# Kernel optimization log

Hardware: AMD Instinct MI355X
Metric: run time of the kernel (lower is better)

Reference implementation:

```python
import jax, jax.numpy as jnp
import numpy as np

N_NODES = 500_000
N_EDGES = 5_000_000


def setup_inputs() -> dict:
    key = jax.random.key(0)
    k_x, k_e, k_w1, k_w2 = jax.random.split(key, 4)
    x = jax.random.normal(k_x, (N_NODES, 1), dtype=jnp.float32)
    edge_index = jax.random.randint(k_e, (2, N_EDGES), 0, N_NODES, dtype=jnp.int32)
    # Glorot-style init, matching PyG GCNConv default scale
    W1 = jax.random.normal(k_w1, (1, 16), dtype=jnp.float32) * np.sqrt(2.0 / (1 + 16))
    b1 = jnp.zeros((16,), dtype=jnp.float32)
    W2 = jax.random.normal(k_w2, (16, 1), dtype=jnp.float32) * np.sqrt(2.0 / (16 + 1))
    b2 = jnp.zeros((1,), dtype=jnp.float32)
    return {"x": x, "W1": W1, "b1": b1, "W2": W2, "b2": b2,
            "edge_index": edge_index}


def reference(x, W1, b1, W2, b2, edge_index):
    n = x.shape[0]
    src, dst = edge_index[0], edge_index[1]
    self_idx = jnp.arange(n, dtype=src.dtype)
    # GCNConv default: add self-loops, symmetric normalization deg^-1/2
    src_f = jnp.concatenate([src, self_idx])  # [E+N]
    dst_f = jnp.concatenate([dst, self_idx])  # [E+N]
    deg = jax.ops.segment_sum(jnp.ones(src_f.shape[0], x.dtype), dst_f,
                              num_segments=n)  # [N]
    dinv = jnp.where(deg > 0, jax.lax.rsqrt(jnp.maximum(deg, 1.0)), 0.0)
    norm = dinv[src_f] * dinv[dst_f]  # [E+N] edge weights

    def gcn_conv(h, W, b):
        h = h @ W  # [N, out]
        msg = h[src_f] * norm[:, None]  # gather + scale, [E+N, out]
        agg = jax.ops.segment_sum(msg, dst_f, num_segments=n)  # scatter-add
        return agg + b

    h = jax.nn.relu(gcn_conv(x, W1, b1))  # [N, 16]
    out = gcn_conv(h, W2, b2)  # [N, 1]
    return out.squeeze(-1)  # [N]
```

## Files before the change

### kernel.cpp

```cpp
#include <hip/hip_runtime.h>

#define N_NODES 500000
#define N_EDGES 5000000
#define NB_C 489
#define PB 512
#define EPB 9768
#define SRC_MASK 0xFFFFFu


__global__ __launch_bounds__(1024)
void hist_kernel(const int* __restrict__ dst, unsigned* __restrict__ hist) {
    __shared__ unsigned h[NB_C];
    for (int i = threadIdx.x; i < NB_C; i += 1024) h[i] = 0u;
    __syncthreads();
    const int b = blockIdx.x;
    const long s0 = (long)b * EPB;
    const int n = (int)min((long)EPB, (long)N_EDGES - s0);
    const int4* d4 = (const int4*)(dst + s0);
    const int n4 = n >> 2;
    for (int i = threadIdx.x; i < n4; i += 1024) {
        int4 d = d4[i];
        atomicAdd(&h[d.x >> 10], 1u);
        atomicAdd(&h[d.y >> 10], 1u);
        atomicAdd(&h[d.z >> 10], 1u);
        atomicAdd(&h[d.w >> 10], 1u);
    }
    __syncthreads();
    unsigned* row = hist + (size_t)b * NB_C;
    for (int i = threadIdx.x; i < NB_C; i += 1024) row[i] = h[i];
}

__global__ __launch_bounds__(512)
void prefix_kernel(unsigned* __restrict__ hist, unsigned* __restrict__ binTotal) {
    __shared__ unsigned A[PB], B[PB];
    const int bin = blockIdx.x;
    const int t = threadIdx.x;
    const unsigned c = hist[(size_t)t * NB_C + bin];
    A[t] = c;
    __syncthreads();
    unsigned* cur = A; unsigned* nxt = B;
    for (int off = 1; off < PB; off <<= 1) {
        nxt[t] = cur[t] + (t >= off ? cur[t - off] : 0u);
        __syncthreads();
        unsigned* tmp = cur; cur = nxt; nxt = tmp;
    }
    hist[(size_t)t * NB_C + bin] = cur[t] - c;
    if (t == PB - 1) binTotal[bin] = cur[PB - 1];
}

__global__ __launch_bounds__(512)
void binscan_kernel(const unsigned* __restrict__ binTotal,
                    unsigned* __restrict__ binStart) {
    __shared__ unsigned A[512], B[512];
    const int t = threadIdx.x;
    A[t] = (t < NB_C) ? binTotal[t] : 0u;
    __syncthreads();
    unsigned* cur = A; unsigned* nxt = B;
    for (int off = 1; off < 512; off <<= 1) {
        nxt[t] = cur[t] + (t >= off ? cur[t - off] : 0u);
        __syncthreads();
        unsigned* tmp = cur; cur = nxt; nxt = tmp;
    }
    if (t < NB_C) binStart[t] = (t == 0) ? 0u : cur[t - 1];
    if (t == 0) binStart[NB_C] = cur[NB_C - 1];
}

__global__ __launch_bounds__(512)
void place_kernel(const int* __restrict__ src, const int* __restrict__ dst,
                  const unsigned* __restrict__ hist,
                  const unsigned* __restrict__ binStart,
                  unsigned* __restrict__ edgebuf) {
    __shared__ unsigned lcnt[NB_C];
    __shared__ unsigned lstart[NB_C];
    __shared__ unsigned gbase[NB_C];
    __shared__ unsigned bump[NB_C];
    __shared__ unsigned scanA[512], scanB[512];
    __shared__ unsigned recs[EPB];

    const int b = blockIdx.x;
    const int t = threadIdx.x;
    const unsigned* row = hist + (size_t)b * NB_C;
    for (int i = t; i < NB_C; i += 512) {
        lcnt[i] = 0u;
        bump[i] = 0u;
        gbase[i] = binStart[i] + row[i];
    }
    __syncthreads();
    const long s0 = (long)b * EPB;
    const int n = (int)min((long)EPB, (long)N_EDGES - s0);
    const int4* d4 = (const int4*)(dst + s0);
    const int4* s4 = (const int4*)(src + s0);
    const int n4 = n >> 2;
    for (int i = t; i < n4; i += 512) {
        int4 d = d4[i];
        atomicAdd(&lcnt[d.x >> 10], 1u);
        atomicAdd(&lcnt[d.y >> 10], 1u);
        atomicAdd(&lcnt[d.z >> 10], 1u);
        atomicAdd(&lcnt[d.w >> 10], 1u);
    }
    __syncthreads();
    scanA[t] = (t < NB_C) ? lcnt[t] : 0u;
    __syncthreads();
    unsigned* cur = scanA; unsigned* nxt = scanB;
    for (int off = 1; off < 512; off <<= 1) {
        nxt[t] = cur[t] + (t >= off ? cur[t - off] : 0u);
        __syncthreads();
        unsigned* tmp = cur; cur = nxt; nxt = tmp;
    }
    if (t < NB_C) lstart[t] = cur[t] - lcnt[t];
    __syncthreads();
    for (int i = t; i < n4; i += 512) {
        int4 s = s4[i];
        int4 d = d4[i];
        unsigned bin, pos;
        bin = (unsigned)d.x >> 10;
        pos = lstart[bin] + atomicAdd(&bump[bin], 1u);
        recs[pos] = ((unsigned)(d.x & 1023) << 20) | (unsigned)s.x;
        bin = (unsigned)d.y >> 10;
        pos = lstart[bin] + atomicAdd(&bump[bin], 1u);
        recs[pos] = ((unsigned)(d.y & 1023) << 20) | (unsigned)s.y;
        bin = (unsigned)d.z >> 10;
        pos = lstart[bin] + atomicAdd(&bump[bin], 1u);
        recs[pos] = ((unsigned)(d.z & 1023) << 20) | (unsigned)s.z;
        bin = (unsigned)d.w >> 10;
        pos = lstart[bin] + atomicAdd(&bump[bin], 1u);
        recs[pos] = ((unsigned)(d.w & 1023) << 20) | (unsigned)s.w;
    }
    __syncthreads();
    const int wave = t >> 6;
    const int lane = t & 63;
    for (int bin = wave; bin < NB_C; bin += 8) {
        const unsigned L  = lcnt[bin];
        const unsigned gs = gbase[bin];
        const unsigned ls = lstart[bin];
        for (unsigned i = lane; i < L; i += 64)
            edgebuf[gs + i] = recs[ls + i];
    }
}

__global__ __launch_bounds__(1024)
void deg_dinv_kernel(const unsigned* __restrict__ edgebuf,
                     const unsigned* __restrict__ binStart,
                     const float* __restrict__ x,
                     float* __restrict__ dinv, float* __restrict__ u) {
    __shared__ unsigned cnt[1024];
    cnt[threadIdx.x] = 0u;
    __syncthreads();
    const int bin = blockIdx.x;
    const unsigned e0 = binStart[bin], e1 = binStart[bin + 1];
    const unsigned ea = (e0 + 3u) & ~3u;
    const unsigned eb = e1 & ~3u;
    for (unsigned e = e0 + threadIdx.x; e < min(ea, e1); e += 1024)
        atomicAdd(&cnt[edgebuf[e] >> 20], 1u);
    if (ea < eb) {
        const uint4* p4 = (const uint4*)(edgebuf + ea);
        const unsigned nv = (eb - ea) >> 2;
        for (unsigned i = threadIdx.x; i < nv; i += 1024) {
            uint4 r = p4[i];
            atomicAdd(&cnt[r.x >> 20], 1u);
            atomicAdd(&cnt[r.y >> 20], 1u);
            atomicAdd(&cnt[r.z >> 20], 1u);
            atomicAdd(&cnt[r.w >> 20], 1u);
        }
    }
    for (unsigned e = max(eb, min(ea, e1)) + threadIdx.x; e < e1; e += 1024)
        atomicAdd(&cnt[edgebuf[e] >> 20], 1u);
    __syncthreads();
    const int node = (bin << 10) + threadIdx.x;
    if (node < N_NODES) {
        float di = rsqrtf((float)cnt[threadIdx.x] + 1.0f);
        dinv[node] = di;
        u[node] = x[node] * di;
    }
}

__global__ __launch_bounds__(1024)
void agg1_kernel(const unsigned* __restrict__ edgebuf,
                 const unsigned* __restrict__ binStart,
                 const float* __restrict__ dinv, const float* __restrict__ u,
                 const float* __restrict__ W1, const float* __restrict__ b1,
                 const float* __restrict__ W2, float* __restrict__ w) {
    __shared__ float sum[1024];
    sum[threadIdx.x] = 0.0f;
    __syncthreads();
    const int bin = blockIdx.x;
    const unsigned e0 = binStart[bin], e1 = binStart[bin + 1];
    const unsigned ea = (e0 + 3u) & ~3u;
    const unsigned eb = e1 & ~3u;
    for (unsigned e = e0 + threadIdx.x; e < min(ea, e1); e += 1024) {
        unsigned rec = edgebuf[e];
        atomicAdd(&sum[rec >> 20], u[rec & SRC_MASK]);
    }
    if (ea < eb) {
        const uint4* p4 = (const uint4*)(edgebuf + ea);
        const unsigned nv = (eb - ea) >> 2;
        for (unsigned i = threadIdx.x; i < nv; i += 1024) {
            uint4 r = p4[i];
            atomicAdd(&sum[r.x >> 20], u[r.x & SRC_MASK]);
            atomicAdd(&sum[r.y >> 20], u[r.y & SRC_MASK]);
            atomicAdd(&sum[r.z >> 20], u[r.z & SRC_MASK]);
            atomicAdd(&sum[r.w >> 20], u[r.w & SRC_MASK]);
        }
    }
    for (unsigned e = max(eb, min(ea, e1)) + threadIdx.x; e < e1; e += 1024) {
        unsigned rec = edgebuf[e];
        atomicAdd(&sum[rec >> 20], u[rec & SRC_MASK]);
    }
    __syncthreads();
    const int node = (bin << 10) + threadIdx.x;
    if (node < N_NODES) {
        float di = dinv[node];
        float s = di * (sum[threadIdx.x] + u[node]);
        float t = 0.0f;
#pragma unroll
        for (int j = 0; j < 16; ++j) {
            float h = fmaf(W1[j], s, b1[j]);
            h = fmaxf(h, 0.0f);
            t = fmaf(h, W2[j], t);
        }
        w[node] = t * di;
    }
}

__global__ __launch_bounds__(1024)
void agg2_kernel(const unsigned* __restrict__ edgebuf,
                 const unsigned* __restrict__ binStart,
                 const float* __restrict__ dinv, const float* __restrict__ w,
                 const float* __restrict__ b2, float* __restrict__ out) {
    __shared__ float sum[1024];
    sum[threadIdx.x] = 0.0f;
    __syncthreads();
    const int bin = blockIdx.x;
    const unsigned e0 = binStart[bin], e1 = binStart[bin + 1];
    const unsigned ea = (e0 + 3u) & ~3u;
    const unsigned eb = e1 & ~3u;
    for (unsigned e = e0 + threadIdx.x; e < min(ea, e1); e += 1024) {
        unsigned rec = edgebuf[e];
        atomicAdd(&sum[rec >> 20], w[rec & SRC_MASK]);
    }
    if (ea < eb) {
        const uint4* p4 = (const uint4*)(edgebuf + ea);
        const unsigned nv = (eb - ea) >> 2;
        for (unsigned i = threadIdx.x; i < nv; i += 1024) {
            uint4 r = p4[i];
            atomicAdd(&sum[r.x >> 20], w[r.x & SRC_MASK]);
            atomicAdd(&sum[r.y >> 20], w[r.y & SRC_MASK]);
            atomicAdd(&sum[r.z >> 20], w[r.z & SRC_MASK]);
            atomicAdd(&sum[r.w >> 20], w[r.w & SRC_MASK]);
        }
    }
    for (unsigned e = max(eb, min(ea, e1)) + threadIdx.x; e < e1; e += 1024) {
        unsigned rec = edgebuf[e];
        atomicAdd(&sum[rec >> 20], w[rec & SRC_MASK]);
    }
    __syncthreads();
    const int node = (bin << 10) + threadIdx.x;
    if (node < N_NODES)
        out[node] = fmaf(dinv[node], sum[threadIdx.x] + w[node], b2[0]);
}

__global__ __launch_bounds__(256)
void deg_kernel(const int* __restrict__ dst, float* __restrict__ deg) {
    const int tid = blockIdx.x * blockDim.x + threadIdx.x;
    const int stride = gridDim.x * blockDim.x;
    const int nvec = N_EDGES / 4;
    const int4* dst4 = (const int4*)dst;
    for (int i = tid; i < nvec; i += stride) {
        int4 d = dst4[i];
        atomicAdd(&deg[d.x], 1.0f);
        atomicAdd(&deg[d.y], 1.0f);
        atomicAdd(&deg[d.z], 1.0f);
        atomicAdd(&deg[d.w], 1.0f);
    }
}
__global__ __launch_bounds__(256)
void node1_kernel(const float* __restrict__ x, float* __restrict__ deg_to_dinv,
                  float* __restrict__ u) {
    const int i = blockIdx.x * blockDim.x + threadIdx.x;
    if (i >= N_NODES) return;
    float di = rsqrtf(deg_to_dinv[i] + 1.0f);
    deg_to_dinv[i] = di;
    u[i] = x[i] * di;
}
__global__ __launch_bounds__(256)
void scatter_kernel(const int* __restrict__ src, const int* __restrict__ dst,
                    const float* __restrict__ val, float* __restrict__ acc) {
    const int tid = blockIdx.x * blockDim.x + threadIdx.x;
    const int stride = gridDim.x * blockDim.x;
    const int nvec = N_EDGES / 4;
    const int4* src4 = (const int4*)src;
    const int4* dst4 = (const int4*)dst;
    for (int i = tid; i < nvec; i += stride) {
        int4 s = src4[i];
        int4 d = dst4[i];
        atomicAdd(&acc[d.x], val[s.x]);
        atomicAdd(&acc[d.y], val[s.y]);
        atomicAdd(&acc[d.z], val[s.z]);
        atomicAdd(&acc[d.w], val[s.w]);
    }
}
__global__ __launch_bounds__(256)
void node2_kernel(const float* __restrict__ dinv, const float* __restrict__ u,
                  const float* __restrict__ acc1, const float* __restrict__ W1,
                  const float* __restrict__ b1, const float* __restrict__ W2,
                  float* __restrict__ w) {
    const int i = blockIdx.x * blockDim.x + threadIdx.x;
    if (i >= N_NODES) return;
    float di = dinv[i];
    float s = di * (acc1[i] + u[i]);
    float t = 0.0f;
#pragma unroll
    for (int j = 0; j < 16; ++j) {
        float h = fmaf(W1[j], s, b1[j]);
        h = fmaxf(h, 0.0f);
        t = fmaf(h, W2[j], t);
    }
    w[i] = t * di;
}
__global__ __launch_bounds__(256)
void final_kernel(const float* __restrict__ dinv, const float* __restrict__ w,
                  const float* __restrict__ acc2, const float* __restrict__ b2,
                  float* __restrict__ out) {
    const int i = blockIdx.x * blockDim.x + threadIdx.x;
    if (i >= N_NODES) return;
    float wi = w[i];
    out[i] = fmaf(dinv[i], acc2[i] + wi, b2[0]);
}

extern "C" void kernel_launch(void* const* d_in, const int* in_sizes, int n_in,
                              void* d_out, int out_size, void* d_ws, size_t ws_size,
                              hipStream_t stream) {
    const float* x  = (const float*)d_in[0];
    const float* W1 = (const float*)d_in[1];
    const float* b1 = (const float*)d_in[2];
    const float* W2 = (const float*)d_in[3];
    const float* b2 = (const float*)d_in[4];
    const int* edge_index = (const int*)d_in[5];
    const int* src = edge_index;
    const int* dst = edge_index + N_EDGES;
    float* out = (float*)d_out;
    char* ws = (char*)d_ws;

    const size_t OFF_EDGEBUF  = 0;
    const size_t OFF_HIST     = 20000000;
    const size_t OFF_BINSTART = 21001472;
    const size_t OFF_BINTOTAL = 21003440;
    const size_t OFF_DINV     = 21005408;
    const size_t OFF_U        = OFF_DINV + 2000000;
    const size_t OFF_W        = OFF_U + 2000000;
    const size_t FAST_WS      = OFF_W + 2000000;

    if (ws_size >= FAST_WS) {
        unsigned* edgebuf  = (unsigned*)(ws + OFF_EDGEBUF);
        unsigned* hist     = (unsigned*)(ws + OFF_HIST);
        unsigned* binStart = (unsigned*)(ws + OFF_BINSTART);
        unsigned* binTotal = (unsigned*)(ws + OFF_BINTOTAL);
        float* dinv = (float*)(ws + OFF_DINV);
        float* u    = (float*)(ws + OFF_U);
        float* w    = (float*)(ws + OFF_W);

        hist_kernel<<<PB, 1024, 0, stream>>>(dst, hist);
        prefix_kernel<<<NB_C, PB, 0, stream>>>(hist, binTotal);
        binscan_kernel<<<1, 512, 0, stream>>>(binTotal, binStart);
        place_kernel<<<PB, 512, 0, stream>>>(src, dst, hist, binStart, edgebuf);
        deg_dinv_kernel<<<NB_C, 1024, 0, stream>>>(edgebuf, binStart, x, dinv, u);
        agg1_kernel<<<NB_C, 1024, 0, stream>>>(edgebuf, binStart, dinv, u, W1, b1, W2, w);
        agg2_kernel<<<NB_C, 1024, 0, stream>>>(edgebuf, binStart, dinv, w, b2, out);
    } else {
        float* buf  = (float*)d_ws;
        float* dinv = buf;
        float* acc1 = buf + 1 * N_NODES;
        float* acc2 = buf + 2 * N_NODES;
        float* u    = buf + 3 * N_NODES;
        float* w    = out;
        hipMemsetAsync(d_ws, 0, 3 * N_NODES * sizeof(float), stream);
        const int nodeBlocks = (N_NODES + 255) / 256;
        const int edgeBlocks = 2048;
        deg_kernel<<<edgeBlocks, 256, 0, stream>>>(dst, dinv);
        node1_kernel<<<nodeBlocks, 256, 0, stream>>>(x, dinv, u);
        scatter_kernel<<<edgeBlocks, 256, 0, stream>>>(src, dst, u, acc1);
        node2_kernel<<<nodeBlocks, 256, 0, stream>>>(dinv, u, acc1, W1, b1, W2, w);
        scatter_kernel<<<edgeBlocks, 256, 0, stream>>>(src, dst, w, acc2);
        final_kernel<<<nodeBlocks, 256, 0, stream>>>(dinv, w, acc2, b2, out);
    }
}
```

Before: 181.9 us.

## Sort edges per destination node into CSR and aggregate without atomics

The degree kernel now also scans per-node counts inside each bin and scatters edge records into a second buffer sorted by destination node, producing per-node row starts. Both aggregation kernels then become one thread per node, summing its row serially with no shared-memory float atomics. The placement kernel reuses the prefix-scanned histogram to get local bin counts instead of recounting, and runs with 1024 threads. The cost is an extra pass over the edges and a second 20MB buffer, plus imbalance and uncoalesced loads from one thread walking each row serially.

```diff
diff --git a/kernel.cpp b/kernel.cpp
--- a/kernel.cpp
+++ b/kernel.cpp
@@ -65,51 +65,43 @@
     if (t == 0) binStart[NB_C] = cur[NB_C - 1];
 }
 
-__global__ __launch_bounds__(512)
+__global__ __launch_bounds__(1024)
 void place_kernel(const int* __restrict__ src, const int* __restrict__ dst,
                   const unsigned* __restrict__ hist,
+                  const unsigned* __restrict__ binTotal,
                   const unsigned* __restrict__ binStart,
                   unsigned* __restrict__ edgebuf) {
-    __shared__ unsigned lcnt[NB_C];
-    __shared__ unsigned lstart[NB_C];
-    __shared__ unsigned gbase[NB_C];
-    __shared__ unsigned bump[NB_C];
-    __shared__ unsigned scanA[512], scanB[512];
+    __shared__ unsigned lcnt[512], lstart[512], gbase[512], bump[512];
+    __shared__ unsigned scanA[1024], scanB[1024];
     __shared__ unsigned recs[EPB];
 
     const int b = blockIdx.x;
     const int t = threadIdx.x;
-    const unsigned* row = hist + (size_t)b * NB_C;
-    for (int i = t; i < NB_C; i += 512) {
-        lcnt[i] = 0u;
-        bump[i] = 0u;
-        gbase[i] = binStart[i] + row[i];
-    }
-    __syncthreads();
-    const long s0 = (long)b * EPB;
-    const int n = (int)min((long)EPB, (long)N_EDGES - s0);
-    const int4* d4 = (const int4*)(dst + s0);
-    const int4* s4 = (const int4*)(src + s0);
-    const int n4 = n >> 2;
-    for (int i = t; i < n4; i += 512) {
-        int4 d = d4[i];
-        atomicAdd(&lcnt[d.x >> 10], 1u);
-        atomicAdd(&lcnt[d.y >> 10], 1u);
-        atomicAdd(&lcnt[d.z >> 10], 1u);
-        atomicAdd(&lcnt[d.w >> 10], 1u);
+    const unsigned* row  = hist + (size_t)b * NB_C;
+    const unsigned* row1 = hist + (size_t)(b + 1) * NB_C;
+    for (int i = t; i < NB_C; i += 1024) {
+        const unsigned p = row[i];
+        lcnt[i]  = (b < PB - 1) ? (row1[i] - p) : (binTotal[i] - p);
+        gbase[i] = binStart[i] + p;
+        bump[i]  = 0u;
     }
     __syncthreads();
     scanA[t] = (t < NB_C) ? lcnt[t] : 0u;
     __syncthreads();
     unsigned* cur = scanA; unsigned* nxt = scanB;
-    for (int off = 1; off < 512; off <<= 1) {
+    for (int off = 1; off < 1024; off <<= 1) {
         nxt[t] = cur[t] + (t >= off ? cur[t - off] : 0u);
         __syncthreads();
         unsigned* tmp = cur; cur = nxt; nxt = tmp;
     }
     if (t < NB_C) lstart[t] = cur[t] - lcnt[t];
     __syncthreads();
-    for (int i = t; i < n4; i += 512) {
+    const long s0 = (long)b * EPB;
+    const int n = (int)min((long)EPB, (long)N_EDGES - s0);
+    const int4* s4 = (const int4*)(src + s0);
+    const int4* d4 = (const int4*)(dst + s0);
+    const int n4 = n >> 2;
+    for (int i = t; i < n4; i += 1024) {
         int4 s = s4[i];
         int4 d = d4[i];
         unsigned bin, pos;
@@ -129,7 +121,7 @@
     __syncthreads();
     const int wave = t >> 6;
     const int lane = t & 63;
-    for (int bin = wave; bin < NB_C; bin += 8) {
+    for (int bin = wave; bin < NB_C; bin += 16) {
         const unsigned L  = lcnt[bin];
         const unsigned gs = gbase[bin];
         const unsigned ls = lstart[bin];
@@ -139,23 +131,28 @@
 }
 
 __global__ __launch_bounds__(1024)
-void deg_dinv_kernel(const unsigned* __restrict__ edgebuf,
+void deg_sort_kernel(const unsigned* __restrict__ edgebuf,
                      const unsigned* __restrict__ binStart,
                      const float* __restrict__ x,
-                     float* __restrict__ dinv, float* __restrict__ u) {
-    __shared__ unsigned cnt[1024];
-    cnt[threadIdx.x] = 0u;
+                     float* __restrict__ dinv, float* __restrict__ u,
+                     unsigned* __restrict__ nstart,
+                     unsigned* __restrict__ edgebuf2) {
+    __shared__ unsigned cnt[1024], ns[1024], bump[1024];
+    __shared__ unsigned scanA[1024], scanB[1024];
+    const int t = threadIdx.x;
+    cnt[t] = 0u;
+    bump[t] = 0u;
     __syncthreads();
     const int bin = blockIdx.x;
     const unsigned e0 = binStart[bin], e1 = binStart[bin + 1];
     const unsigned ea = (e0 + 3u) & ~3u;
     const unsigned eb = e1 & ~3u;
-    for (unsigned e = e0 + threadIdx.x; e < min(ea, e1); e += 1024)
+    for (unsigned e = e0 + t; e < min(ea, e1); e += 1024)
         atomicAdd(&cnt[edgebuf[e] >> 20], 1u);
     if (ea < eb) {
         const uint4* p4 = (const uint4*)(edgebuf + ea);
         const unsigned nv = (eb - ea) >> 2;
-        for (unsigned i = threadIdx.x; i < nv; i += 1024) {
+        for (unsigned i = t; i < nv; i += 1024) {
             uint4 r = p4[i];
             atomicAdd(&cnt[r.x >> 20], 1u);
             atomicAdd(&cnt[r.y >> 20], 1u);
@@ -163,100 +160,70 @@
             atomicAdd(&cnt[r.w >> 20], 1u);
         }
     }
-    for (unsigned e = max(eb, min(ea, e1)) + threadIdx.x; e < e1; e += 1024)
+    for (unsigned e = max(eb, min(ea, e1)) + t; e < e1; e += 1024)
         atomicAdd(&cnt[edgebuf[e] >> 20], 1u);
     __syncthreads();
-    const int node = (bin << 10) + threadIdx.x;
+    scanA[t] = cnt[t];
+    __syncthreads();
+    unsigned* cur = scanA; unsigned* nxt = scanB;
+    for (int off = 1; off < 1024; off <<= 1) {
+        nxt[t] = cur[t] + (t >= off ? cur[t - off] : 0u);
+        __syncthreads();
+        unsigned* tmp = cur; cur = nxt; nxt = tmp;
+    }
+    ns[t] = cur[t] - cnt[t];
+    const int node = (bin << 10) + t;
+    nstart[node] = e0 + ns[t];
     if (node < N_NODES) {
-        float di = rsqrtf((float)cnt[threadIdx.x] + 1.0f);
+        float di = rsqrtf((float)cnt[t] + 1.0f);
         dinv[node] = di;
         u[node] = x[node] * di;
     }
-}
-
-__global__ __launch_bounds__(1024)
-void agg1_kernel(const unsigned* __restrict__ edgebuf,
-                 const unsigned* __restrict__ binStart,
+    __syncthreads();
+    for (unsigned e = e0 + t; e < e1; e += 1024) {
+        const unsigned rec = edgebuf[e];
+        const unsigned l = rec >> 20;
+        const unsigned pos = ns[l] + atomicAdd(&bump[l], 1u);
+        edgebuf2[e0 + pos] = rec;
+    }
+}
+
+__global__ __launch_bounds__(1024)
+void agg1_kernel(const unsigned* __restrict__ edgebuf2,
+                 const unsigned* __restrict__ nstart,
                  const float* __restrict__ dinv, const float* __restrict__ u,
                  const float* __restrict__ W1, const float* __restrict__ b1,
                  const float* __restrict__ W2, float* __restrict__ w) {
-    __shared__ float sum[1024];
-    sum[threadIdx.x] = 0.0f;
-    __syncthreads();
-    const int bin = blockIdx.x;
-    const unsigned e0 = binStart[bin], e1 = binStart[bin + 1];
-    const unsigned ea = (e0 + 3u) & ~3u;
-    const unsigned eb = e1 & ~3u;
-    for (unsigned e = e0 + threadIdx.x; e < min(ea, e1); e += 1024) {
-        unsigned rec = edgebuf[e];
-        atomicAdd(&sum[rec >> 20], u[rec & SRC_MASK]);
-    }
-    if (ea < eb) {
-        const uint4* p4 = (const uint4*)(edgebuf + ea);
-        const unsigned nv = (eb - ea) >> 2;
-        for (unsigned i = threadIdx.x; i < nv; i += 1024) {
-            uint4 r = p4[i];
-            atomicAdd(&sum[r.x >> 20], u[r.x & SRC_MASK]);
-            atomicAdd(&sum[r.y >> 20], u[r.y & SRC_MASK]);
-            atomicAdd(&sum[r.z >> 20], u[r.z & SRC_MASK]);
-            atomicAdd(&sum[r.w >> 20], u[r.w & SRC_MASK]);
-        }
-    }
-    for (unsigned e = max(eb, min(ea, e1)) + threadIdx.x; e < e1; e += 1024) {
-        unsigned rec = edgebuf[e];
-        atomicAdd(&sum[rec >> 20], u[rec & SRC_MASK]);
-    }
-    __syncthreads();
-    const int node = (bin << 10) + threadIdx.x;
-    if (node < N_NODES) {
-        float di = dinv[node];
-        float s = di * (sum[threadIdx.x] + u[node]);
-        float t = 0.0f;
+    const int node = blockIdx.x * 1024 + threadIdx.x;
+    if (node >= N_NODES) return;
+    const unsigned rs = nstart[node], re = nstart[node + 1];
+    float acc = 0.0f;
+    for (unsigned e = rs; e < re; ++e)
+        acc += u[edgebuf2[e] & SRC_MASK];
+    const float di = dinv[node];
+    const float s = di * (acc + u[node]);
+    float tt = 0.0f;
 #pragma unroll
-        for (int j = 0; j < 16; ++j) {
-            float h = fmaf(W1[j], s, b1[j]);
-            h = fmaxf(h, 0.0f);
-            t = fmaf(h, W2[j], t);
-        }
-        w[node] = t * di;
-    }
-}
-
-__global__ __launch_bounds__(1024)
-void agg2_kernel(const unsigned* __restrict__ edgebuf,
-                 const unsigned* __restrict__ binStart,
+    for (int j = 0; j < 16; ++j) {
+        float h = fmaf(W1[j], s, b1[j]);
+        h = fmaxf(h, 0.0f);
+        tt = fmaf(h, W2[j], tt);
+    }
+    w[node] = tt * di;
+}
+
+__global__ __launch_bounds__(1024)
+void agg2_kernel(const unsigned* __restrict__ edgebuf2,
+                 const unsigned* __restrict__ nstart,
                  const float* __restrict__ dinv, const float* __restrict__ w,
                  const float* __restrict__ b2, float* __restrict__ out) {
-    __shared__ float sum[1024];
-    sum[threadIdx.x] = 0.0f;
-    __syncthreads();
-    const int bin = blockIdx.x;
-    const unsigned e0 = binStart[bin], e1 = binStart[bin + 1];
-    const unsigned ea = (e0 + 3u) & ~3u;
-    const unsigned eb = e1 & ~3u;
-    for (unsigned e = e0 + threadIdx.x; e < min(ea, e1); e += 1024) {
-        unsigned rec = edgebuf[e];
-        atomicAdd(&sum[rec >> 20], w[rec & SRC_MASK]);
-    }
-    if (ea < eb) {
-        const uint4* p4 = (const uint4*)(edgebuf + ea);
-        const unsigned nv = (eb - ea) >> 2;
-        for (unsigned i = threadIdx.x; i < nv; i += 1024) {
-            uint4 r = p4[i];
-            atomicAdd(&sum[r.x >> 20], w[r.x & SRC_MASK]);
-            atomicAdd(&sum[r.y >> 20], w[r.y & SRC_MASK]);
-            atomicAdd(&sum[r.z >> 20], w[r.z & SRC_MASK]);
-            atomicAdd(&sum[r.w >> 20], w[r.w & SRC_MASK]);
-        }
-    }
-    for (unsigned e = max(eb, min(ea, e1)) + threadIdx.x; e < e1; e += 1024) {
-        unsigned rec = edgebuf[e];
-        atomicAdd(&sum[rec >> 20], w[rec & SRC_MASK]);
-    }
-    __syncthreads();
-    const int node = (bin << 10) + threadIdx.x;
-    if (node < N_NODES)
-        out[node] = fmaf(dinv[node], sum[threadIdx.x] + w[node], b2[0]);
+    const int node = blockIdx.x * 1024 + threadIdx.x;
+    if (node >= N_NODES) return;
+    const unsigned rs = nstart[node], re = nstart[node + 1];
+    float acc = 0.0f;
+    for (unsigned e = rs; e < re; ++e)
+        acc += w[edgebuf2[e] & SRC_MASK];
+    out[node] = fmaf(dinv[node], acc + w[node], b2[0]);
 }
 
 __global__ __launch_bounds__(256)
@@ -345,27 +312,33 @@
     const size_t OFF_HIST     = 20000000;
     const size_t OFF_BINSTART = 21001472;
     const size_t OFF_BINTOTAL = 21003440;
-    const size_t OFF_DINV     = 21005408;
-    const size_t OFF_U        = OFF_DINV + 2000000;
-    const size_t OFF_W        = OFF_U + 2000000;
-    const size_t FAST_WS      = OFF_W + 2000000;
+    const size_t OFF_NSTART   = 21005408;
+    const size_t OFF_DINV     = 23008352;
+    const size_t OFF_U        = 25008352;
+    const size_t OFF_W        = 27008352;
+    const size_t OFF_EDGEBUF2 = 29008352;
+    const size_t FAST_WS      = 49008352;
 
     if (ws_size >= FAST_WS) {
         unsigned* edgebuf  = (unsigned*)(ws + OFF_EDGEBUF);
         unsigned* hist     = (unsigned*)(ws + OFF_HIST);
         unsigned* binStart = (unsigned*)(ws + OFF_BINSTART);
         unsigned* binTotal = (unsigned*)(ws + OFF_BINTOTAL);
+        unsigned* nstart   = (unsigned*)(ws + OFF_NSTART);
         float* dinv = (float*)(ws + OFF_DINV);
         float* u    = (float*)(ws + OFF_U);
         float* w    = (float*)(ws + OFF_W);
+        unsigned* edgebuf2 = (unsigned*)(ws + OFF_EDGEBUF2);
 
         hist_kernel<<<PB, 1024, 0, stream>>>(dst, hist);
         prefix_kernel<<<NB_C, PB, 0, stream>>>(hist, binTotal);
         binscan_kernel<<<1, 512, 0, stream>>>(binTotal, binStart);
-        place_kernel<<<PB, 512, 0, stream>>>(src, dst, hist, binStart, edgebuf);
-        deg_dinv_kernel<<<NB_C, 1024, 0, stream>>>(edgebuf, binStart, x, dinv, u);
-        agg1_kernel<<<NB_C, 1024, 0, stream>>>(edgebuf, binStart, dinv, u, W1, b1, W2, w);
-        agg2_kernel<<<NB_C, 1024, 0, stream>>>(edgebuf, binStart, dinv, w, b2, out);
+        place_kernel<<<PB, 1024, 0, stream>>>(src, dst, hist, binTotal, binStart, edgebuf);
+        deg_sort_kernel<<<NB_C, 1024, 0, stream>>>(edgebuf, binStart, x, dinv, u,
+                                                   nstart, edgebuf2);
+        agg1_kernel<<<NB_C, 1024, 0, stream>>>(edgebuf2, nstart, dinv, u,
+                                               W1, b1, W2, w);
+        agg2_kernel<<<NB_C, 1024, 0, stream>>>(edgebuf2, nstart, dinv, w, b2, out);
     } else {
         float* buf  = (float*)d_ws;
         float* dinv = buf;
```

Result: slower. 227.7 us (+25.2%).
